# Performance work log

Measured on AMD Instinct MI355X. Metric: run time of the kernel, lower is better.

## Reference

```python
import jax, jax.numpy as jnp
import numpy as np

V_MIN = -10.0
V_MAX = 10.0
NUM_ATOMS = 251
B = 131072
N_OBS = 128
N_ACT = 32
HID = 512


def _ln(x, g, b, eps=1e-5):
    m = jnp.mean(x, axis=-1, keepdims=True)
    v = jnp.var(x, axis=-1, keepdims=True)
    return (x - m) * jax.lax.rsqrt(v + eps) * g + b


def setup_inputs() -> dict:
    key = jax.random.key(0)
    ks = jax.random.split(key, 16)

    def lin(k, fi, fo):
        kw, kb = jax.random.split(k)
        lim = 1.0 / np.sqrt(fi)
        W = jax.random.uniform(kw, (fi, fo), jnp.float32, -lim, lim)
        b = jax.random.uniform(kb, (fo,), jnp.float32, -lim, lim)
        return W, b

    W1, b1 = lin(ks[0], N_OBS + N_ACT, HID)
    W2, b2 = lin(ks[1], HID, HID // 2)
    W3, b3 = lin(ks[2], HID // 2, HID // 4)
    W4, b4 = lin(ks[3], HID // 4, NUM_ATOMS)

    return {
        "obs": jax.random.normal(ks[4], (B, N_OBS), jnp.float32),
        "actions": jax.random.normal(ks[5], (B, N_ACT), jnp.float32),
        "rewards": jax.random.normal(ks[6], (B,), jnp.float32),
        "bootstrap": (jax.random.uniform(ks[7], (B,)) > 0.05).astype(jnp.float32),
        "discount": jnp.full((B,), 0.99, jnp.float32),
        "q_support": jnp.linspace(V_MIN, V_MAX, NUM_ATOMS, dtype=jnp.float32),
        "W1": W1, "b1": b1, "g1": jnp.ones((HID,), jnp.float32), "be1": jnp.zeros((HID,), jnp.float32),
        "W2": W2, "b2": b2, "g2": jnp.ones((HID // 2,), jnp.float32), "be2": jnp.zeros((HID // 2,), jnp.float32),
        "W3": W3, "b3": b3, "g3": jnp.ones((HID // 4,), jnp.float32), "be3": jnp.zeros((HID // 4,), jnp.float32),
        "W4": W4, "b4": b4,
    }


def _net(obs, actions, W1, b1, g1, be1, W2, b2, g2, be2, W3, b3, g3, be3, W4, b4):
    x = jnp.concatenate([obs, actions], axis=1)
    x = jax.nn.silu(_ln(x @ W1 + b1, g1, be1))
    x = jax.nn.silu(_ln(x @ W2 + b2, g2, be2))
    x = jax.nn.silu(_ln(x @ W3 + b3, g3, be3))
    return x @ W4 + b4  # [B, NUM_ATOMS] logits


def reference(obs, actions, rewards, bootstrap, discount, q_support,
              W1, b1, g1, be1, W2, b2, g2, be2, W3, b3, g3, be3, W4, b4):
    # C51 categorical projection (DistributionalQNetwork.projection)
    delta_z = (V_MAX - V_MIN) / (NUM_ATOMS - 1)
    bsz = rewards.shape[0]
    target_z = rewards[:, None] + bootstrap[:, None] * discount[:, None] * q_support[None, :]
    target_z = jnp.clip(target_z, V_MIN, V_MAX)
    b = (target_z - V_MIN) / delta_z  # fractional bin positions [B, A]
    lower = jnp.floor(b).astype(jnp.int32)
    upper = jnp.ceil(b).astype(jnp.int32)
    is_integer = upper == lower
    lower_mask = (lower > 0) & is_integer
    upper_mask = (lower == 0) & is_integer
    lower = jnp.where(lower_mask, lower - 1, lower)
    upper = jnp.where(upper_mask, upper + 1, upper)

    logits = _net(obs, actions, W1, b1, g1, be1, W2, b2, g2, be2, W3, b3, g3, be3, W4, b4)
    next_dist = jax.nn.softmax(logits, axis=1)

    offset = (jnp.arange(bsz, dtype=jnp.int32) * NUM_ATOMS)[:, None]  # [B,1]
    max_index = bsz * NUM_ATOMS - 1
    li = jnp.clip((lower + offset).reshape(-1), 0, max_index)
    ui = jnp.clip((upper + offset).reshape(-1), 0, max_index)

    w_lo = (next_dist * (upper.astype(jnp.float32) - b)).reshape(-1)
    w_hi = (next_dist * (b - lower.astype(jnp.float32))).reshape(-1)

    proj = jnp.zeros((bsz * NUM_ATOMS,), next_dist.dtype)
    proj = proj.at[li].add(w_lo).at[ui].add(w_hi)
    return proj.reshape(bsz, NUM_ATOMS)
```

## Files before the change

### kernel.cpp

```cpp
#include <hip/hip_runtime.h>


#define THREADS 256
#define PREP_THREADS 256

typedef __attribute__((ext_vector_type(8))) short short8v;
typedef __attribute__((ext_vector_type(4))) float f32x4;

__device__ __forceinline__ unsigned short f2bf(float f) {
  union { float f; unsigned u; } v; v.f = f;
  unsigned u = v.u;
  u += 0x7fffu + ((u >> 16) & 1u);
  return (unsigned short)(u >> 16);
}
__device__ __forceinline__ unsigned pack2bf(float a, float b) {
  unsigned r;
  asm("v_cvt_pk_bf16_f32 %0, %1, %2" : "=v"(r) : "v"(a), "v"(b));
  return r;
}

__global__ void prep_kernel(const float* __restrict__ W1, const float* __restrict__ W2,
                            const float* __restrict__ W3, const float* __restrict__ W4,
                            unsigned short* __restrict__ ws) {
  int i = blockIdx.x * PREP_THREADS + threadIdx.x;
  if (i < 81920) {
    int n = i / 160, k = i - n * 160;
    ws[i] = f2bf(W1[k * 512 + n]);
  } else if (i < 212992) {
    int j = i - 81920; int n = j >> 9, k = j & 511;
    ws[i] = f2bf(W2[k * 256 + n]);
  } else if (i < 245760) {
    int j = i - 212992; int n = j >> 8, k = j & 255;
    ws[i] = f2bf(W3[k * 128 + n]);
  } else if (i < 278528) {
    int j = i - 245760; int n = j >> 7, k = j & 127;
    ws[i] = (n < 251) ? f2bf(W4[k * 251 + n]) : (unsigned short)0;
  }
}

#define OFF_R   0
#define OFF_ZS  32768
#define OFF_B4  33792
#define OFF_RED 34816
#define LDS_TOTAL 36096

template<int KD, int NFT>
__device__ __forceinline__ void gemm_rolled(const unsigned short* __restrict__ WT,
                                            const unsigned char* __restrict__ Hb,
                                            int fbase, f32x4 (&acc)[NFT][2]) {
  constexpr int KS = KD / 32;
  const int lane = threadIdx.x & 63;
  const int lm = lane & 15, kg = lane >> 4;
  const unsigned short* wp = WT + (fbase + lm) * KD + kg * 8;
  int bbase[2], bswz[2];
#pragma unroll
  for (int rt = 0; rt < 2; ++rt) {
    const int r = rt * 16 + lm;
    bbase[rt] = r * (KD * 2) + kg * 16;
    bswz[rt] = (r & 7) << 4;
  }
  short8v A0[NFT], A1[NFT], B0[2], B1[2];

  auto loadA = [&](short8v (&A)[NFT], int k) {
#pragma unroll
    for (int ft = 0; ft < NFT; ++ft)
      A[ft] = *(const short8v*)(wp + ft * (16 * KD) + k * 32);
  };
  auto loadB = [&](short8v (&B)[2], int k) {
#pragma unroll
    for (int rt = 0; rt < 2; ++rt)
      B[rt] = *(const short8v*)(Hb + ((bbase[rt] + k * 64) ^ bswz[rt]));
  };
  auto domfma = [&](short8v (&A)[NFT], short8v (&B)[2]) {
#pragma unroll
    for (int ft = 0; ft < NFT; ++ft) {
      acc[ft][0] = __builtin_amdgcn_mfma_f32_16x16x32_bf16(A[ft], B[0], acc[ft][0], 0, 0, 0);
      acc[ft][1] = __builtin_amdgcn_mfma_f32_16x16x32_bf16(A[ft], B[1], acc[ft][1], 0, 0, 0);
    }
  };

  loadA(A0, 0); loadB(B0, 0);
  if constexpr ((KS & 1) == 0) {
#pragma unroll 1
    for (int ks = 0; ks < KS - 2; ks += 2) {
      loadA(A1, ks + 1); loadB(B1, ks + 1);
      domfma(A0, B0);
      loadA(A0, ks + 2); loadB(B0, ks + 2);
      domfma(A1, B1);
    }
    loadA(A1, KS - 1); loadB(B1, KS - 1);
    domfma(A0, B0);
    domfma(A1, B1);
  } else {
#pragma unroll 1
    for (int ks = 0; ks < KS - 1; ks += 2) {
      loadA(A1, ks + 1); loadB(B1, ks + 1);
      domfma(A0, B0);
      loadA(A0, ks + 2); loadB(B0, ks + 2);
      domfma(A1, B1);
    }
    domfma(A0, B0);
  }
}

template<int ND, int NFT>
__device__ __forceinline__ void ln_silu_store(
    f32x4 (&acc)[NFT][2],
    const float* __restrict__ bias, const float* __restrict__ g,
    const float* __restrict__ be, unsigned char* __restrict__ Hb,
    float* __restrict__ redL, int fbase, int fq)
{
  const int lane = threadIdx.x & 63;
  const int lm = lane & 15, kg = lane >> 4;
  float s[2] = {0.f, 0.f}, q[2] = {0.f, 0.f};
#pragma unroll
  for (int ft = 0; ft < NFT; ++ft) {
    const int f0 = fbase + ft * 16 + kg * 4;
    const f32x4 bb = *(const f32x4*)(bias + f0);
#pragma unroll
    for (int rt = 0; rt < 2; ++rt)
#pragma unroll
      for (int rg = 0; rg < 4; ++rg) {
        float x = acc[ft][rt][rg] + bb[rg];
        acc[ft][rt][rg] = x;
        s[rt] += x; q[rt] += x * x;
      }
  }
#pragma unroll
  for (int rt = 0; rt < 2; ++rt) {
    s[rt] += __shfl_xor(s[rt], 16); s[rt] += __shfl_xor(s[rt], 32);
    q[rt] += __shfl_xor(q[rt], 16); q[rt] += __shfl_xor(q[rt], 32);
  }
  if (lane < 16) {
#pragma unroll
    for (int rt = 0; rt < 2; ++rt) {
      redL[(rt * 16 + lm) * 9 + fq * 2    ] = s[rt];
      redL[(rt * 16 + lm) * 9 + fq * 2 + 1] = q[rt];
    }
  }
  __syncthreads();
  float mean[2], rstd[2];
#pragma unroll
  for (int rt = 0; rt < 2; ++rt) {
    const int row = rt * 16 + lm;
    float S = 0.f, Q = 0.f;
#pragma unroll
    for (int w = 0; w < 4; ++w) {
      S += redL[row * 9 + w * 2];
      Q += redL[row * 9 + w * 2 + 1];
    }
    float m = S * (1.0f / ND);
    float v = Q * (1.0f / ND) - m * m;
    mean[rt] = m; rstd[rt] = rsqrtf(v + 1e-5f);
  }
#pragma unroll
  for (int ft = 0; ft < NFT; ++ft) {
    const int f0 = fbase + ft * 16 + kg * 4;
    const f32x4 g4 = *(const f32x4*)(g + f0);
    const f32x4 e4 = *(const f32x4*)(be + f0);
#pragma unroll
    for (int rt = 0; rt < 2; ++rt) {
      const int row = rt * 16 + lm;
      float h[4];
#pragma unroll
      for (int rg = 0; rg < 4; ++rg) {
        float y = (acc[ft][rt][rg] - mean[rt]) * rstd[rt] * g4[rg] + e4[rg];
        h[rg] = y * (1.0f / (1.0f + __expf(-y)));
      }
      uint2 w; w.x = pack2bf(h[0], h[1]); w.y = pack2bf(h[2], h[3]);
      int byte = row * (ND * 2) + f0 * 2;
      byte ^= ((row & 7) << 4);
      *(uint2*)(Hb + byte) = w;
    }
  }
}

__global__ __launch_bounds__(THREADS, 4) void fused_kernel(
    const float* __restrict__ obs, const float* __restrict__ actions,
    const float* __restrict__ rewards, const float* __restrict__ bootstrap,
    const float* __restrict__ discount, const float* __restrict__ q_support,
    const float* __restrict__ b1, const float* __restrict__ g1, const float* __restrict__ be1,
    const float* __restrict__ b2, const float* __restrict__ g2, const float* __restrict__ be2,
    const float* __restrict__ b3, const float* __restrict__ g3, const float* __restrict__ be3,
    const float* __restrict__ b4,
    const unsigned short* __restrict__ ws,
    float* __restrict__ out)
{
  __shared__ __align__(16) unsigned char smem[LDS_TOTAL];
  const int tid  = threadIdx.x;
  const int fq   = tid >> 6;
  const int lane = tid & 63;
  const int lm   = lane & 15;
  const int kg   = lane >> 4;
  const int row0 = blockIdx.x * 32;

  const unsigned short* W1T = ws;
  const unsigned short* W2T = ws + 81920;
  const unsigned short* W3T = ws + 212992;
  const unsigned short* W4T = ws + 245760;

  float* zsL  = (float*)(smem + OFF_ZS);
  float* b4L  = (float*)(smem + OFF_B4);
  float* redL = (float*)(smem + OFF_RED);

  float rw[2], bt[2], dc[2];
#pragma unroll
  for (int rt = 0; rt < 2; ++rt) {
    const int r = row0 + rt * 16 + lm;
    rw[rt] = rewards[r]; bt[rt] = bootstrap[r]; dc[rt] = discount[r];
  }

  zsL[tid] = (tid < 251) ? q_support[tid] : 0.f;
  b4L[tid] = (tid < 251) ? b4[tid] : 0.f;

  {
    unsigned char* Xb = smem + OFF_R;
#pragma unroll 1
    for (int it = 0; it < 5; ++it) {
      const int qq = it * THREADS + tid;
      const int r  = qq / 40;
      const int c4 = (qq - r * 40) * 4;
      float4 v;
      if (c4 < 128) v = *(const float4*)(obs + (size_t)(row0 + r) * 128 + c4);
      else          v = *(const float4*)(actions + (size_t)(row0 + r) * 32 + (c4 - 128));
      uint2 w; w.x = pack2bf(v.x, v.y); w.y = pack2bf(v.z, v.w);
      int byte = r * 320 + c4 * 2;
      byte ^= ((r & 7) << 4);
      *(uint2*)(Xb + byte) = w;
    }
  }
  __syncthreads();

  f32x4 acc1[8][2];
#pragma unroll
  for (int i = 0; i < 8; ++i) { acc1[i][0] = f32x4{0,0,0,0}; acc1[i][1] = f32x4{0,0,0,0}; }
  gemm_rolled<160, 8>(W1T, smem + OFF_R, fq * 128, acc1);
  ln_silu_store<512, 8>(acc1, b1, g1, be1, smem + OFF_R, redL, fq * 128, fq);
  __syncthreads();

  f32x4 acc2[4][2];
#pragma unroll
  for (int i = 0; i < 4; ++i) { acc2[i][0] = f32x4{0,0,0,0}; acc2[i][1] = f32x4{0,0,0,0}; }
  gemm_rolled<512, 4>(W2T, smem + OFF_R, fq * 64, acc2);
  ln_silu_store<256, 4>(acc2, b2, g2, be2, smem + OFF_R, redL, fq * 64, fq);
  __syncthreads();

  f32x4 acc3[2][2];
#pragma unroll
  for (int i = 0; i < 2; ++i) { acc3[i][0] = f32x4{0,0,0,0}; acc3[i][1] = f32x4{0,0,0,0}; }
  gemm_rolled<256, 2>(W3T, smem + OFF_R, fq * 32, acc3);
  ln_silu_store<128, 2>(acc3, b3, g3, be3, smem + OFF_R, redL, fq * 32, fq);
  __syncthreads();

  f32x4 acc4[4][2];
#pragma unroll
  for (int i = 0; i < 4; ++i) { acc4[i][0] = f32x4{0,0,0,0}; acc4[i][1] = f32x4{0,0,0,0}; }
  gemm_rolled<128, 4>(W4T, smem + OFF_R, fq * 64, acc4);

  float lv[4][2][4];
#pragma unroll
  for (int ft = 0; ft < 4; ++ft) {
    const int f0 = fq * 64 + ft * 16 + kg * 4;
    const f32x4 bb = *(const f32x4*)(b4L + f0);
#pragma unroll
    for (int rt = 0; rt < 2; ++rt)
#pragma unroll
      for (int rg = 0; rg < 4; ++rg) {
        const int f = f0 + rg;
        lv[ft][rt][rg] = (f < 251) ? (acc4[ft][rt][rg] + bb[rg]) : -1e30f;
      }
  }

#pragma unroll
  for (int rt = 0; rt < 2; ++rt) {
    float m = lv[0][rt][0];
#pragma unroll
    for (int ft = 0; ft < 4; ++ft)
#pragma unroll
      for (int rg = 0; rg < 4; ++rg) m = fmaxf(m, lv[ft][rt][rg]);
    m = fmaxf(m, __shfl_xor(m, 16));
    m = fmaxf(m, __shfl_xor(m, 32));
    if (lane < 16) redL[(rt * 16 + lm) * 5 + fq] = m;
  }
  __syncthreads();

  float* projL = (float*)(smem + OFF_R);
  for (int i = tid; i < 32 * 251; i += THREADS) projL[i] = 0.f;

  float gm[2];
#pragma unroll
  for (int rt = 0; rt < 2; ++rt) {
    const int row = rt * 16 + lm;
    float m = redL[row * 5];
#pragma unroll
    for (int w = 1; w < 4; ++w) m = fmaxf(m, redL[row * 5 + w]);
    gm[rt] = m;
  }
  __syncthreads();
#pragma unroll
  for (int rt = 0; rt < 2; ++rt) {
    float E = 0.f;
#pragma unroll
    for (int ft = 0; ft < 4; ++ft)
#pragma unroll
      for (int rg = 0; rg < 4; ++rg) {
        float e = __expf(lv[ft][rt][rg] - gm[rt]);
        lv[ft][rt][rg] = e;
        E += e;
      }
    E += __shfl_xor(E, 16); E += __shfl_xor(E, 32);
    if (lane < 16) redL[(rt * 16 + lm) * 5 + fq] = E;
  }
  __syncthreads();
  float inv[2];
#pragma unroll
  for (int rt = 0; rt < 2; ++rt) {
    const int row = rt * 16 + lm;
    float E = 0.f;
#pragma unroll
    for (int w = 0; w < 4; ++w) E += redL[row * 5 + w];
    inv[rt] = 1.0f / E;
  }

  constexpr float DZF = 20.0f / 250.0f;
  constexpr float INVDZ = 1.0f / DZF;
#pragma unroll
  for (int ft = 0; ft < 4; ++ft) {
    const int f0 = fq * 64 + ft * 16 + kg * 4;
    const f32x4 z4 = *(const f32x4*)(zsL + f0);
#pragma unroll
    for (int rt = 0; rt < 2; ++rt) {
      const int base = (rt * 16 + lm) * 251;
      const float bd = __fmul_rn(bt[rt], dc[rt]);
#pragma unroll
      for (int rg = 0; rg < 4; ++rg) {
        const int f = f0 + rg;
        if (f < 251) {
          const float p = lv[ft][rt][rg] * inv[rt];
          float t = __fadd_rn(rw[rt], __fmul_rn(bd, z4[rg]));
          t = fminf(fmaxf(t, -10.0f), 10.0f);
          const float bfr = __fmul_rn(__fsub_rn(t, -10.0f), INVDZ);
          const float fl = floorf(bfr), fu = ceilf(bfr);
          int l = (int)fl, u = (int)fu;
          if (fl == fu) { if (l > 0) --l; else ++u; }
          atomicAdd(projL + base + l, p * ((float)u - bfr));
          atomicAdd(projL + base + u, p * (bfr - (float)l));
        }
      }
    }
  }
  __syncthreads();

  const float4* ps = (const float4*)projL;
  float4* po = (float4*)(out + (size_t)row0 * 251);
  for (int i = tid; i < 2008; i += THREADS) po[i] = ps[i];
}

extern "C" void kernel_launch(void* const* d_in, const int* in_sizes, int n_in,
                              void* d_out, int out_size, void* d_ws, size_t ws_size,
                              hipStream_t stream) {
  const float* obs  = (const float*)d_in[0];
  const float* act  = (const float*)d_in[1];
  const float* rew  = (const float*)d_in[2];
  const float* boot = (const float*)d_in[3];
  const float* disc = (const float*)d_in[4];
  const float* zs   = (const float*)d_in[5];
  const float* W1   = (const float*)d_in[6];
  const float* b1   = (const float*)d_in[7];
  const float* g1   = (const float*)d_in[8];
  const float* be1  = (const float*)d_in[9];
  const float* W2   = (const float*)d_in[10];
  const float* b2   = (const float*)d_in[11];
  const float* g2   = (const float*)d_in[12];
  const float* be2  = (const float*)d_in[13];
  const float* W3   = (const float*)d_in[14];
  const float* b3   = (const float*)d_in[15];
  const float* g3   = (const float*)d_in[16];
  const float* be3  = (const float*)d_in[17];
  const float* W4   = (const float*)d_in[18];
  const float* b4   = (const float*)d_in[19];
  unsigned short* wsp = (unsigned short*)d_ws;

  const int Bn = in_sizes[2];
  prep_kernel<<<(278528 + PREP_THREADS - 1) / PREP_THREADS, PREP_THREADS, 0, stream>>>(
      W1, W2, W3, W4, wsp);
  fused_kernel<<<Bn / 32, THREADS, 0, stream>>>(obs, act, rew, boot, disc, zs,
      b1, g1, be1, b2, g2, be2, b3, g3, be3, b4, wsp, (float*)d_out);
}
```

Baseline: 483.1 us.

## Split fused MLP kernel into per-layer kernels with global bf16 intermediates

Replaces the single fused per-tile kernel with four layer kernels (L1, L2, L3, L4+softmax+projection) that pass bf16 activation tiles through workspace memory, processed in row chunks sized to the available workspace. The aim is to let each stage use smaller register and LDS footprints and higher occupancy than the monolithic kernel. The cost is extra global writes and reads of the intermediates plus more kernel launches. Whether this path runs depends on workspace size, and the fused kernel is kept as a fallback.

```diff
diff --git a/kernel.cpp b/kernel.cpp
--- a/kernel.cpp
+++ b/kernel.cpp
@@ -38,12 +38,6 @@
   }
 }
 
-#define OFF_R   0
-#define OFF_ZS  32768
-#define OFF_B4  33792
-#define OFF_RED 34816
-#define LDS_TOTAL 36096
-
 template<int KD, int NFT>
 __device__ __forceinline__ void gemm_rolled(const unsigned short* __restrict__ WT,
                                             const unsigned char* __restrict__ Hb,
@@ -60,7 +54,6 @@
     bswz[rt] = (r & 7) << 4;
   }
   short8v A0[NFT], A1[NFT], B0[2], B1[2];
-
   auto loadA = [&](short8v (&A)[NFT], int k) {
 #pragma unroll
     for (int ft = 0; ft < NFT; ++ft)
@@ -78,7 +71,6 @@
       acc[ft][1] = __builtin_amdgcn_mfma_f32_16x16x32_bf16(A[ft], B[1], acc[ft][1], 0, 0, 0);
     }
   };
-
   loadA(A0, 0); loadB(B0, 0);
   if constexpr ((KS & 1) == 0) {
 #pragma unroll 1
@@ -174,6 +166,232 @@
     }
   }
 }
+
+template<int NU4>
+__device__ __forceinline__ void tile_flush(const unsigned char* R, unsigned short* g) {
+  const uint4* s = (const uint4*)R;
+  uint4* d = (uint4*)g;
+  for (int i = threadIdx.x; i < NU4; i += THREADS) d[i] = s[i];
+}
+template<int NU4>
+__device__ __forceinline__ void tile_stage(unsigned char* R, const unsigned short* g) {
+  const uint4* s = (const uint4*)g;
+  uint4* d = (uint4*)R;
+  for (int i = threadIdx.x; i < NU4; i += THREADS) d[i] = s[i];
+}
+
+__global__ __launch_bounds__(THREADS, 4) void kA(
+    const float* __restrict__ obs, const float* __restrict__ actions,
+    const float* __restrict__ b1, const float* __restrict__ g1,
+    const float* __restrict__ be1, const unsigned short* __restrict__ ws,
+    unsigned short* __restrict__ H1, int row_base)
+{
+  __shared__ __align__(16) unsigned char smem[32768 + 1152];
+  unsigned char* R = smem;
+  float* redL = (float*)(smem + 32768);
+  const int tid = threadIdx.x, fq = tid >> 6;
+  const int row0 = row_base + blockIdx.x * 32;
+
+#pragma unroll 1
+  for (int it = 0; it < 5; ++it) {
+    const int qq = it * THREADS + tid;
+    const int r  = qq / 40;
+    const int c4 = (qq - r * 40) * 4;
+    float4 v;
+    if (c4 < 128) v = *(const float4*)(obs + (size_t)(row0 + r) * 128 + c4);
+    else          v = *(const float4*)(actions + (size_t)(row0 + r) * 32 + (c4 - 128));
+    uint2 w; w.x = pack2bf(v.x, v.y); w.y = pack2bf(v.z, v.w);
+    int byte = r * 320 + c4 * 2;
+    byte ^= ((r & 7) << 4);
+    *(uint2*)(R + byte) = w;
+  }
+  __syncthreads();
+
+  f32x4 acc[8][2];
+#pragma unroll
+  for (int i = 0; i < 8; ++i) { acc[i][0] = f32x4{0,0,0,0}; acc[i][1] = f32x4{0,0,0,0}; }
+  gemm_rolled<160, 8>(ws, R, fq * 128, acc);
+  ln_silu_store<512, 8>(acc, b1, g1, be1, R, redL, fq * 128, fq);
+  __syncthreads();
+  tile_flush<2048>(R, H1 + (size_t)blockIdx.x * (32 * 512));
+}
+
+__global__ __launch_bounds__(THREADS, 4) void kB(
+    const float* __restrict__ b2, const float* __restrict__ g2,
+    const float* __restrict__ be2, const unsigned short* __restrict__ ws,
+    const unsigned short* __restrict__ H1, unsigned short* __restrict__ H2)
+{
+  __shared__ __align__(16) unsigned char smem[32768 + 1152];
+  unsigned char* R = smem;
+  float* redL = (float*)(smem + 32768);
+  const int tid = threadIdx.x, fq = tid >> 6;
+  tile_stage<2048>(R, H1 + (size_t)blockIdx.x * (32 * 512));
+  __syncthreads();
+  f32x4 acc[4][2];
+#pragma unroll
+  for (int i = 0; i < 4; ++i) { acc[i][0] = f32x4{0,0,0,0}; acc[i][1] = f32x4{0,0,0,0}; }
+  gemm_rolled<512, 4>(ws + 81920, R, fq * 64, acc);
+  ln_silu_store<256, 4>(acc, b2, g2, be2, R, redL, fq * 64, fq);
+  __syncthreads();
+  tile_flush<1024>(R, H2 + (size_t)blockIdx.x * (32 * 256));
+}
+
+__global__ __launch_bounds__(THREADS, 4) void kC(
+    const float* __restrict__ b3, const float* __restrict__ g3,
+    const float* __restrict__ be3, const unsigned short* __restrict__ ws,
+    const unsigned short* __restrict__ H2, unsigned short* __restrict__ H3)
+{
+  __shared__ __align__(16) unsigned char smem[16384 + 1152];
+  unsigned char* R = smem;
+  float* redL = (float*)(smem + 16384);
+  const int tid = threadIdx.x, fq = tid >> 6;
+  tile_stage<1024>(R, H2 + (size_t)blockIdx.x * (32 * 256));
+  __syncthreads();
+  f32x4 acc[2][2];
+#pragma unroll
+  for (int i = 0; i < 2; ++i) { acc[i][0] = f32x4{0,0,0,0}; acc[i][1] = f32x4{0,0,0,0}; }
+  gemm_rolled<256, 2>(ws + 212992, R, fq * 32, acc);
+  ln_silu_store<128, 2>(acc, b3, g3, be3, R, redL, fq * 32, fq);
+  __syncthreads();
+  tile_flush<512>(R, H3 + (size_t)blockIdx.x * (32 * 128));
+}
+
+__global__ __launch_bounds__(THREADS, 4) void kD(
+    const float* __restrict__ rewards, const float* __restrict__ bootstrap,
+    const float* __restrict__ discount, const float* __restrict__ q_support,
+    const float* __restrict__ b4, const unsigned short* __restrict__ ws,
+    const unsigned short* __restrict__ H3, float* __restrict__ out, int row_base)
+{
+  __shared__ __align__(16) unsigned char smem[32128 + 1024 + 1024 + 640];
+  unsigned char* R = smem;
+  float* zsL  = (float*)(smem + 32128);
+  float* b4L  = (float*)(smem + 33152);
+  float* redL = (float*)(smem + 34176);
+  const int tid = threadIdx.x, fq = tid >> 6;
+  const int lane = tid & 63, lm = lane & 15, kg = lane >> 4;
+  const int row0 = row_base + blockIdx.x * 32;
+
+  zsL[tid] = (tid < 251) ? q_support[tid] : 0.f;
+  b4L[tid] = (tid < 251) ? b4[tid] : 0.f;
+  tile_stage<512>(R, H3 + (size_t)blockIdx.x * (32 * 128));
+  __syncthreads();
+
+  f32x4 acc4[4][2];
+#pragma unroll
+  for (int i = 0; i < 4; ++i) { acc4[i][0] = f32x4{0,0,0,0}; acc4[i][1] = f32x4{0,0,0,0}; }
+  gemm_rolled<128, 4>(ws + 245760, R, fq * 64, acc4);
+
+  float rw[2], bt[2], dc[2];
+#pragma unroll
+  for (int rt = 0; rt < 2; ++rt) {
+    const int r = row0 + rt * 16 + lm;
+    rw[rt] = rewards[r]; bt[rt] = bootstrap[r]; dc[rt] = discount[r];
+  }
+
+  float lv[4][2][4];
+#pragma unroll
+  for (int ft = 0; ft < 4; ++ft) {
+    const int f0 = fq * 64 + ft * 16 + kg * 4;
+    const f32x4 bb = *(const f32x4*)(b4L + f0);
+#pragma unroll
+    for (int rt = 0; rt < 2; ++rt)
+#pragma unroll
+      for (int rg = 0; rg < 4; ++rg) {
+        const int f = f0 + rg;
+        lv[ft][rt][rg] = (f < 251) ? (acc4[ft][rt][rg] + bb[rg]) : -1e30f;
+      }
+  }
+
+#pragma unroll
+  for (int rt = 0; rt < 2; ++rt) {
+    float m = lv[0][rt][0];
+#pragma unroll
+    for (int ft = 0; ft < 4; ++ft)
+#pragma unroll
+      for (int rg = 0; rg < 4; ++rg) m = fmaxf(m, lv[ft][rt][rg]);
+    m = fmaxf(m, __shfl_xor(m, 16));
+    m = fmaxf(m, __shfl_xor(m, 32));
+    if (lane < 16) redL[(rt * 16 + lm) * 5 + fq] = m;
+  }
+  __syncthreads();
+
+  float* projL = (float*)R;
+  for (int i = tid; i < 32 * 251; i += THREADS) projL[i] = 0.f;
+
+  float gm[2];
+#pragma unroll
+  for (int rt = 0; rt < 2; ++rt) {
+    const int row = rt * 16 + lm;
+    float m = redL[row * 5];
+#pragma unroll
+    for (int w = 1; w < 4; ++w) m = fmaxf(m, redL[row * 5 + w]);
+    gm[rt] = m;
+  }
+  __syncthreads();
+#pragma unroll
+  for (int rt = 0; rt < 2; ++rt) {
+    float E = 0.f;
+#pragma unroll
+    for (int ft = 0; ft < 4; ++ft)
+#pragma unroll
+      for (int rg = 0; rg < 4; ++rg) {
+        float e = __expf(lv[ft][rt][rg] - gm[rt]);
+        lv[ft][rt][rg] = e;
+        E += e;
+      }
+    E += __shfl_xor(E, 16); E += __shfl_xor(E, 32);
+    if (lane < 16) redL[(rt * 16 + lm) * 5 + fq] = E;
+  }
+  __syncthreads();
+  float inv[2];
+#pragma unroll
+  for (int rt = 0; rt < 2; ++rt) {
+    const int row = rt * 16 + lm;
+    float E = 0.f;
+#pragma unroll
+    for (int w = 0; w < 4; ++w) E += redL[row * 5 + w];
+    inv[rt] = 1.0f / E;
+  }
+
+  constexpr float DZF = 20.0f / 250.0f;
+  constexpr float INVDZ = 1.0f / DZF;
+#pragma unroll
+  for (int ft = 0; ft < 4; ++ft) {
+    const int f0 = fq * 64 + ft * 16 + kg * 4;
+    const f32x4 z4 = *(const f32x4*)(zsL + f0);
+#pragma unroll
+    for (int rt = 0; rt < 2; ++rt) {
+      const int base = (rt * 16 + lm) * 251;
+      const float bd = __fmul_rn(bt[rt], dc[rt]);
+#pragma unroll
+      for (int rg = 0; rg < 4; ++rg) {
+        const int f = f0 + rg;
+        if (f < 251) {
+          const float p = lv[ft][rt][rg] * inv[rt];
+          float t = __fadd_rn(rw[rt], __fmul_rn(bd, z4[rg]));
+          t = fminf(fmaxf(t, -10.0f), 10.0f);
+          const float bfr = __fmul_rn(__fsub_rn(t, -10.0f), INVDZ);
+          const float fl = floorf(bfr), fu = ceilf(bfr);
+          int l = (int)fl, u = (int)fu;
+          if (fl == fu) { if (l > 0) --l; else ++u; }
+          atomicAdd(projL + base + l, p * ((float)u - bfr));
+          atomicAdd(projL + base + u, p * (bfr - (float)l));
+        }
+      }
+    }
+  }
+  __syncthreads();
+
+  const float4* ps = (const float4*)projL;
+  float4* po = (float4*)(out + (size_t)row0 * 251);
+  for (int i = tid; i < 2008; i += THREADS) po[i] = ps[i];
+}
+
+#define OFF_R   0
+#define OFF_ZS  32768
+#define OFF_B4  33792
+#define OFF_RED 34816
+#define LDS_TOTAL 36096
 
 __global__ __launch_bounds__(THREADS, 4) void fused_kernel(
     const float* __restrict__ obs, const float* __restrict__ actions,
@@ -209,7 +427,6 @@
     const int r = row0 + rt * 16 + lm;
     rw[rt] = rewards[r]; bt[rt] = bootstrap[r]; dc[rt] = discount[r];
   }
-
   zsL[tid] = (tid < 251) ? q_support[tid] : 0.f;
   b4L[tid] = (tid < 251) ? b4[tid] : 0.f;
 
@@ -384,6 +601,27 @@
   const int Bn = in_sizes[2];
   prep_kernel<<<(278528 + PREP_THREADS - 1) / PREP_THREADS, PREP_THREADS, 0, stream>>>(
       W1, W2, W3, W4, wsp);
-  fused_kernel<<<Bn / 32, THREADS, 0, stream>>>(obs, act, rew, boot, disc, zs,
-      b1, g1, be1, b2, g2, be2, b3, g3, be3, b4, wsp, (float*)d_out);
-}
+
+  long long rcap = ((long long)ws_size - 557056LL - 4096LL) / 1792LL;
+  long long Rc = rcap < 0 ? 0 : rcap;
+  if (Rc > Bn) Rc = Bn;
+  Rc &= ~31LL;
+
+  if (Rc >= 16384) {
+    unsigned short* H1 = wsp + 278528;
+    unsigned short* H2 = H1 + (size_t)Rc * 512;
+    unsigned short* H3 = H2 + (size_t)Rc * 256;
+    for (int base = 0; base < Bn; base += (int)Rc) {
+      const int rows = (Bn - base < (int)Rc) ? (Bn - base) : (int)Rc;
+      const int nb = rows / 32;
+      kA<<<nb, THREADS, 0, stream>>>(obs, act, b1, g1, be1, wsp, H1, base);
+      kB<<<nb, THREADS, 0, stream>>>(b2, g2, be2, wsp, H1, H2);
+      kC<<<nb, THREADS, 0, stream>>>(b3, g3, be3, wsp, H2, H3);
+      kD<<<nb, THREADS, 0, stream>>>(rew, boot, disc, zs, b4, wsp, H3,
+                                     (float*)d_out, base);
+    }
+  } else {
+    fused_kernel<<<Bn / 32, THREADS, 0, stream>>>(obs, act, rew, boot, disc, zs,
+        b1, g1, be1, b2, g2, be2, b3, g3, be3, b4, wsp, (float*)d_out);
+  }
+}
```

Result: slower. 636.0 us (+31.7%).
